# Kernel tuning notes

Measured on AMD Instinct MI355X. Metric: run time of the kernel, lower is better.

The kernel has to match this reference:

```python
import jax, jax.numpy as jnp
import numpy as np

B, S, D, H = 2, 2048, 2048, 16
DH = D // H  # 128


def _rope_tables(seq_len, head_dim, base=10000.0):
    inv_freq = 1.0 / (base ** (jnp.arange(0, head_dim, 2, dtype=jnp.float32) / head_dim))
    t = jnp.arange(seq_len, dtype=jnp.float32)
    freqs = jnp.outer(t, inv_freq)                      # [S, DH/2]
    emb = jnp.concatenate([freqs, freqs], axis=-1)      # [S, DH]
    return jnp.cos(emb), jnp.sin(emb)


def _rotate_half(x):
    x1, x2 = jnp.split(x, 2, axis=-1)
    return jnp.concatenate([-x2, x1], axis=-1)


def setup_inputs() -> dict:
    key = jax.random.key(0)
    ks = jax.random.split(key, 5)
    sc = 0.02
    return {
        "hidden_states": jax.random.normal(ks[0], (B, S, D), jnp.float32),
        "Wq": jax.random.normal(ks[1], (D, D), jnp.float32) * sc,
        "Wk": jax.random.normal(ks[2], (D, D), jnp.float32) * sc,
        "Wv": jax.random.normal(ks[3], (D, D), jnp.float32) * sc,
        "Wo": jax.random.normal(ks[4], (D, D), jnp.float32) * sc,
        "medical_bias": jnp.zeros((1, H, 1, 1), jnp.float32),
    }


def reference(hidden_states, Wq, Wk, Wv, Wo, medical_bias):
    b, s, _ = hidden_states.shape
    # torch Linear: y = x @ W.T  (W is [out, in])
    def proj(x, W):
        y = jnp.einsum('bsd,ed->bse', x, W)
        return y.reshape(b, s, H, DH).transpose(0, 2, 1, 3)  # [b,H,s,DH]

    q = proj(hidden_states, Wq)
    k = proj(hidden_states, Wk)
    v = proj(hidden_states, Wv)

    cos, sin = _rope_tables(s, DH)                 # [s, DH]
    cos = cos[None, None]                          # [1,1,s,DH]
    sin = sin[None, None]
    q = q * cos + _rotate_half(q) * sin
    k = k * cos + _rotate_half(k) * sin

    scores = jnp.einsum('bhqd,bhkd->bhqk', q, k) / jnp.sqrt(jnp.float32(DH))
    scores = scores + medical_bias                 # learned per-head bias
    probs = jax.nn.softmax(scores, axis=-1)
    out = jnp.einsum('bhqk,bhkd->bhqd', probs, v)  # [b,H,s,DH]
    out = out.transpose(0, 2, 1, 3).reshape(b, s, D)
    return jnp.einsum('bsd,ed->bse', out, Wo)
```

## Files before the change

kernel.cpp:

```cpp
#include <hip/hip_runtime.h>
#include <stdint.h>


#define B_ 2
#define S_ 2048
#define D_ 2048
#define H_ 16

typedef float f32x4 __attribute__((ext_vector_type(4)));
typedef short s16x8 __attribute__((ext_vector_type(8)));

__device__ __forceinline__ unsigned short f2bf(float f) {
  union { float f; uint32_t u; } c; c.f = f;
  return (unsigned short)((c.u + 0x7fffu + ((c.u >> 16) & 1u)) >> 16);
}

#define FAST_EXP2(x) __builtin_amdgcn_exp2f(x)

__device__ __forceinline__ void gld_lds16(const void* g, void* l) {
  __builtin_amdgcn_global_load_lds(
      (const __attribute__((address_space(1))) uint32_t*)g,
      (__attribute__((address_space(3))) uint32_t*)l, 16, 0, 0);
}

__global__ __launch_bounds__(256) void k_f2bf_all(
    const float* __restrict__ hs, const float* __restrict__ wq,
    const float* __restrict__ wk, const float* __restrict__ wv,
    const float* __restrict__ wo, unsigned short* __restrict__ hb,
    unsigned short* __restrict__ wall) {
  const int NH = 2097152, NW = 1048576;
  int i = blockIdx.x * 256 + threadIdx.x;
  const int stride = gridDim.x * 256;
  for (; i < NH + 4 * NW; i += stride) {
    f32x4 v;
    ushort4* dst;
    if (i < NH) {
      v = ((const f32x4*)hs)[i];
      dst = (ushort4*)hb + i;
    } else {
      const int j = i - NH;
      const int rgn = j >> 20;
      const int o = j & (NW - 1);
      const float* s = (rgn == 0) ? wq : (rgn == 1) ? wk : (rgn == 2) ? wv : wo;
      v = ((const f32x4*)s)[o];
      dst = (ushort4*)wall + j;
    }
    ushort4 u;
    u.x = f2bf(v.x); u.y = f2bf(v.y); u.z = f2bf(v.z); u.w = f2bf(v.w);
    *dst = u;
  }
}

__global__ __launch_bounds__(256) void k_tab(float2* __restrict__ t2) {
  int t = blockIdx.x * 256 + threadIdx.x;
  int s = t >> 6, j = t & 63;
  float inv = expf(-(float)j * (1.0f / 64.0f) * 9.210340371976184f);
  float sv, cv;
  sincosf((float)s * inv, &sv, &cv);
  t2[t] = float2{cv, sv};
}

__global__ __launch_bounds__(256, 2) void k_gemm(
    const unsigned short* __restrict__ A,
    const unsigned short* __restrict__ W0,
    const unsigned short* __restrict__ W1,
    const unsigned short* __restrict__ W2,
    float* __restrict__ C0,
    unsigned short* __restrict__ Qo,
    unsigned short* __restrict__ Ko,
    unsigned short* __restrict__ VT,
    const float2* __restrict__ tab,
    int plain) {
  __shared__ unsigned short Al[2][128 * 64];
  __shared__ unsigned short Bl[2][128 * 64];

  const int l0 = ((int)blockIdx.z * 32 + (int)blockIdx.y) * 16 + (int)blockIdx.x;
  const int qx = ((int)gridDim.z * 512) >> 3;
  const int wg = (l0 & 7) * qx + (l0 >> 3);
  const int z = wg >> 9;
  const unsigned short* __restrict__ Wp = (z == 0) ? W0 : (z == 1) ? W1 : W2;

  const int tid = threadIdx.x;
  const int w = tid >> 6;
  const int l = tid & 63;
  const int row0 = ((wg >> 4) & 31) * 128;
  const int col0 = (wg & 15) * 128;

  const int c16 = l & 15, g = l >> 4;
  const int cx = c16 & 7;

  const int srow = l >> 3;
  const int sslot = (l & 7) ^ (l >> 3);
  const int scol = sslot << 3;

  int kbase[2];
#pragma unroll
  for (int kk = 0; kk < 2; ++kk)
    kbase[kk] = c16 * 128 + (((kk * 4 + g) ^ cx) << 4);
  const char* AW0 = (const char*)&Al[0][0] + w * 4096;
  const char* AW1 = (const char*)&Al[1][0] + w * 4096;
  const char* BB0 = (const char*)&Bl[0][0];
  const char* BB1 = (const char*)&Bl[1][0];

  f32x4 acc[2][8];
#pragma unroll
  for (int m = 0; m < 2; ++m)
#pragma unroll
    for (int n = 0; n < 8; ++n)
      acc[m][n] = f32x4{0.f, 0.f, 0.f, 0.f};

#define STAGE_G(K0, BUF)                                                       \
  do {                                                                         \
    _Pragma("unroll") for (int i = 0; i < 4; ++i) {                            \
      const int jj = (w << 2) + i;                                             \
      gld_lds16(&A[(size_t)(row0 + (jj << 3) + srow) * 2048 + (K0) + scol],    \
                &Al[BUF][jj * 512]);                                           \
      gld_lds16(&Wp[(size_t)(col0 + (jj << 3) + srow) * 2048 + (K0) + scol],   \
                &Bl[BUF][jj * 512]);                                           \
    }                                                                          \
  } while (0)

#define COMPUTE_G(AW, BBp)                                                     \
  do {                                                                         \
    _Pragma("unroll") for (int kk = 0; kk < 2; ++kk) {                         \
      s16x8 a[2], b[8];                                                        \
      _Pragma("unroll") for (int m = 0; m < 2; ++m)                            \
          a[m] = *(const s16x8*)((AW) + m * 2048 + kbase[kk]);                 \
      _Pragma("unroll") for (int n = 0; n < 8; ++n)                            \
          b[n] = *(const s16x8*)((BBp) + n * 2048 + kbase[kk]);                \
      __builtin_amdgcn_s_setprio(1);                                           \
      _Pragma("unroll") for (int m = 0; m < 2; ++m)                            \
          _Pragma("unroll") for (int n = 0; n < 8; ++n)                        \
              acc[m][n] = __builtin_amdgcn_mfma_f32_16x16x32_bf16(             \
                  a[m], b[n], acc[m][n], 0, 0, 0);                             \
      __builtin_amdgcn_s_setprio(0);                                           \
    }                                                                          \
  } while (0)

  STAGE_G(0, 0);
  __syncthreads();
  for (int k0 = 0; k0 < 2048; k0 += 128) {
    STAGE_G(k0 + 64, 1);
    COMPUTE_G(AW0, BB0);
    __syncthreads();
    if (k0 + 128 < 2048) STAGE_G(k0 + 128, 0);
    COMPUTE_G(AW1, BB1);
    __syncthreads();
  }
#undef STAGE_G
#undef COMPUTE_G

  if (plain) {
#pragma unroll
    for (int m = 0; m < 2; ++m) {
      const int gr = row0 + w * 32 + m * 16 + g * 4;
#pragma unroll
      for (int n = 0; n < 8; ++n) {
        const int gc = col0 + n * 16 + c16;
#pragma unroll
        for (int r = 0; r < 4; ++r)
          C0[(size_t)(gr + r) * 2048 + gc] = acc[m][n][r];
      }
    }
  } else if (z == 2) {
#pragma unroll
    for (int m = 0; m < 2; ++m) {
      const int gr = row0 + w * 32 + m * 16 + g * 4;
      const int b_ = gr >> 11, s_ = gr & 2047;
#pragma unroll
      for (int n = 0; n < 8; ++n) {
        const int gc = col0 + n * 16 + c16;
        ushort4 o;
        o.x = f2bf(acc[m][n][0]);
        o.y = f2bf(acc[m][n][1]);
        o.z = f2bf(acc[m][n][2]);
        o.w = f2bf(acc[m][n][3]);
        *(ushort4*)&VT[((size_t)(b_ * 2048 + gc)) * 2048 + s_] = o;
      }
    }
  } else {
    unsigned short* __restrict__ O = z ? Ko : Qo;
    const float sc = z ? 1.0f : (0.08838834764831845f * 1.4426950408889634f);
#pragma unroll
    for (int m = 0; m < 2; ++m) {
#pragma unroll
      for (int r = 0; r < 4; ++r) {
        const int gr = row0 + w * 32 + m * 16 + g * 4 + r;
        const int s_ = gr & 2047;
#pragma unroll
        for (int n = 0; n < 4; ++n) {
          const float2 f = tab[s_ * 64 + n * 16 + c16];
          const float x1 = acc[m][n][r], x2 = acc[m][n + 4][r];
          O[(size_t)gr * 2048 + col0 + n * 16 + c16] =
              f2bf((x1 * f.x - x2 * f.y) * sc);
          O[(size_t)gr * 2048 + col0 + 64 + n * 16 + c16] =
              f2bf((x2 * f.x + x1 * f.y) * sc);
        }
      }
    }
  }
}

__global__ __launch_bounds__(256, 2) void k_attn(
    const unsigned short* __restrict__ Qb,
    const unsigned short* __restrict__ Kb,
    const unsigned short* __restrict__ Vt,
    unsigned short* __restrict__ Ob) {
  __shared__ unsigned short Kl[2][64 * 128];
  __shared__ unsigned short Vl[2][128 * 64];
  __shared__ unsigned short Pl[4][32 * 64];

  const int l0 = (int)blockIdx.y * 16 + (int)blockIdx.x;
  const int wg = (l0 & 7) * 64 + (l0 >> 3);
  const int bh = wg >> 4;
  const int b = bh >> 4, h = bh & 15;

  const int tid = threadIdx.x, w = tid >> 6, l = tid & 63;
  const int q0 = (wg & 15) * 128 + w * 32;
  const int g = l >> 4, c16 = l & 15;
  const int cx = c16 & 7;

  int kaddr[4], vaddr[2];
#pragma unroll
  for (int kc = 0; kc < 4; ++kc)
    kaddr[kc] = c16 * 256 + ((((kc * 4 + g) ^ cx)) << 4);
#pragma unroll
  for (int kc2 = 0; kc2 < 2; ++kc2)
    vaddr[kc2] = c16 * 128 + ((((kc2 * 4 + g) ^ cx)) << 4);
  const char* PW = (const char*)&Pl[w][0];

  s16x8 qf[2][4];
#pragma unroll
  for (int qq = 0; qq < 2; ++qq)
#pragma unroll
    for (int kc = 0; kc < 4; ++kc)
      qf[qq][kc] = *(const s16x8*)&Qb[(size_t)(b * 2048 + q0 + qq * 16 + c16) * 2048 +
                                      h * 128 + kc * 32 + g * 8];

  f32x4 oacc[2][8];
  float mrow[2][4], lrow[2][4];
#pragma unroll
  for (int qq = 0; qq < 2; ++qq) {
#pragma unroll
    for (int df = 0; df < 8; ++df) oacc[qq][df] = f32x4{0.f, 0.f, 0.f, 0.f};
#pragma unroll
    for (int r = 0; r < 4; ++r) { mrow[qq][r] = -INFINITY; lrow[qq][r] = 0.f; }
  }

#define STAGE(T, BUF)                                                          \
  do {                                                                         \
    _Pragma("unroll") for (int i = 0; i < 4; ++i) {                            \
      const int jj = (w << 2) + i;                                             \
      const int krow = jj * 4 + (l >> 4);                                      \
      const int kslot = (l & 15) ^ (krow & 7);                                 \
      gld_lds16(&Kb[(size_t)(b * 2048 + (T) + krow) * 2048 + h * 128 +        \
                    (kslot << 3)],                                             \
                &Kl[BUF][jj * 512]);                                           \
      const int vrow = jj * 8 + (l >> 3);                                      \
      const int vslot = (l & 7) ^ (vrow & 7);                                  \
      gld_lds16(&Vt[(size_t)(bh * 128 + vrow) * 2048 + (T) + (vslot << 3)],    \
                &Vl[BUF][jj * 512]);                                           \
    }                                                                          \
  } while (0)

#define COMPUTE(BUF_)                                                          \
  do {                                                                         \
    f32x4 sacc[2][4];                                                          \
    _Pragma("unroll") for (int qq = 0; qq < 2; ++qq)                           \
        _Pragma("unroll") for (int n = 0; n < 4; ++n)                          \
            sacc[qq][n] = f32x4{0.f, 0.f, 0.f, 0.f};                           \
    const char* KB = (const char*)&Kl[BUF_][0];                                \
    __builtin_amdgcn_s_setprio(1);                                             \
    _Pragma("unroll") for (int kc = 0; kc < 4; ++kc) {                         \
      s16x8 kb[4];                                                             \
      _Pragma("unroll") for (int n = 0; n < 4; ++n)                            \
          kb[n] = *(const s16x8*)(KB + kaddr[kc] + n * 4096);                  \
      _Pragma("unroll") for (int qq = 0; qq < 2; ++qq)                         \
          _Pragma("unroll") for (int n = 0; n < 4; ++n)                        \
              sacc[qq][n] = __builtin_amdgcn_mfma_f32_16x16x32_bf16(           \
                  qf[qq][kc], kb[n], sacc[qq][n], 0, 0, 0);                    \
    }                                                                          \
    __builtin_amdgcn_s_setprio(0);                                             \
            \
    float mx4[2][4];                                                           \
    float need = 0.f;                                                          \
    _Pragma("unroll") for (int qq = 0; qq < 2; ++qq)                           \
        _Pragma("unroll") for (int r = 0; r < 4; ++r) {                        \
      mx4[qq][r] = fmaxf(fmaxf(sacc[qq][0][r], sacc[qq][1][r]),                \
                         fmaxf(sacc[qq][2][r], sacc[qq][3][r]));               \
      need = fmaxf(need, mx4[qq][r] - mrow[qq][r]);                            \
    }                                                                          \
    if (!__all(need <= 8.0f)) {          \
      _Pragma("unroll") for (int qq = 0; qq < 2; ++qq)                         \
          _Pragma("unroll") for (int r = 0; r < 4; ++r) {                      \
        float mx = mx4[qq][r];                                                 \
        mx = fmaxf(mx, __shfl_xor(mx, 1));                                     \
        mx = fmaxf(mx, __shfl_xor(mx, 2));                                     \
        mx = fmaxf(mx, __shfl_xor(mx, 4));                                     \
        mx = fmaxf(mx, __shfl_xor(mx, 8));                                     \
        float mnew = fmaxf(mrow[qq][r], mx);                                   \
        float alpha = FAST_EXP2(mrow[qq][r] - mnew);                           \
        mrow[qq][r] = mnew;                                                    \
        lrow[qq][r] *= alpha;                                                  \
        _Pragma("unroll") for (int df = 0; df < 8; ++df)                       \
            oacc[qq][df][r] *= alpha;                                          \
      }                                                                        \
    }                                                                          \
    _Pragma("unroll") for (int qq = 0; qq < 2; ++qq) {                         \
      _Pragma("unroll") for (int r = 0; r < 4; ++r) {                          \
        float rs = 0.f;                                                        \
        _Pragma("unroll") for (int n = 0; n < 4; ++n) {                        \
          float p = FAST_EXP2(sacc[qq][n][r] - mrow[qq][r]);                   \
          sacc[qq][n][r] = p;                                                  \
          rs += p;                                                             \
        }                                                                      \
        lrow[qq][r] += rs;                                                     \
      }                                                                        \
      _Pragma("unroll") for (int n = 0; n < 4; ++n)                            \
          _Pragma("unroll") for (int r = 0; r < 4; ++r) {                      \
        const int prow = qq * 16 + g * 4 + r;                                  \
        const int psl = (n * 2 + (c16 >> 3)) ^ (prow & 7);                     \
        Pl[w][prow * 64 + (psl << 3) + (c16 & 7)] = f2bf(sacc[qq][n][r]);      \
      }                                                                        \
    }                                                                          \
    const char* VB = (const char*)&Vl[BUF_][0];                                \
    __builtin_amdgcn_s_setprio(1);                                             \
    _Pragma("unroll") for (int kc2 = 0; kc2 < 2; ++kc2) {                      \
      s16x8 pa[2];                                                             \
      pa[0] = *(const s16x8*)(PW + vaddr[kc2]);                                \
      pa[1] = *(const s16x8*)(PW + vaddr[kc2] + 2048);                         \
      _Pragma("unroll") for (int df = 0; df < 8; ++df) {                       \
        s16x8 vb = *(const s16x8*)(VB + vaddr[kc2] + df * 2048);               \
        oacc[0][df] = __builtin_amdgcn_mfma_f32_16x16x32_bf16(pa[0], vb,       \
                                                              oacc[0][df], 0, 0, 0); \
        oacc[1][df] = __builtin_amdgcn_mfma_f32_16x16x32_bf16(pa[1], vb,       \
                                                              oacc[1][df], 0, 0, 0); \
      }                                                                        \
    }                                                                          \
    __builtin_amdgcn_s_setprio(0);                                             \
  } while (0)

  STAGE(0, 0);
  __syncthreads();
  for (int t = 0; t < 2048; t += 128) {
    STAGE(t + 64, 1);
    COMPUTE(0);
    __syncthreads();
    if (t + 128 < 2048) STAGE(t + 128, 0);
    COMPUTE(1);
    __syncthreads();
  }
#undef STAGE
#undef COMPUTE

#pragma unroll
  for (int qq = 0; qq < 2; ++qq)
#pragma unroll
    for (int r = 0; r < 4; ++r) {
      float tot = lrow[qq][r];
      tot += __shfl_xor(tot, 1);
      tot += __shfl_xor(tot, 2);
      tot += __shfl_xor(tot, 4);
      tot += __shfl_xor(tot, 8);
      const float inv = 1.0f / tot;
      const int srow_ = q0 + qq * 16 + g * 4 + r;
#pragma unroll
      for (int df = 0; df < 8; ++df)
        Ob[(size_t)(b * 2048 + srow_) * 2048 + h * 128 + df * 16 + c16] =
            f2bf(oacc[qq][df][r] * inv);
    }
}

extern "C" void kernel_launch(void* const* d_in, const int* in_sizes, int n_in,
                              void* d_out, int out_size, void* d_ws, size_t ws_size,
                              hipStream_t stream) {
  const float* hs = (const float*)d_in[0];
  const float* Wq = (const float*)d_in[1];
  const float* Wk = (const float*)d_in[2];
  const float* Wv = (const float*)d_in[3];
  const float* Wo = (const float*)d_in[4];
  float* out = (float*)d_out;
  char* ws = (char*)d_ws;

  unsigned short* hb   = (unsigned short*)(ws + 0);
  unsigned short* wall = (unsigned short*)(ws + 16777216);
  unsigned short* wqb  = wall;
  unsigned short* wkb  = wall + 4194304;
  unsigned short* wvb  = wall + 8388608;
  unsigned short* wob  = wall + 12582912;
  unsigned short* Qbb  = (unsigned short*)(ws + 50331648);
  unsigned short* Kbb  = (unsigned short*)(ws + 67108864);
  unsigned short* Vt   = (unsigned short*)(ws + 83886080);
  float2*         tab2 = (float2*)(ws + 100663296);
  unsigned short* Ob   = hb;

  k_f2bf_all<<<2048, 256, 0, stream>>>(hs, Wq, Wk, Wv, Wo, hb, wall);
  k_tab<<<512, 256, 0, stream>>>(tab2);

  k_gemm<<<dim3(16, 32, 3), 256, 0, stream>>>(hb, wqb, wkb, wvb, nullptr, Qbb,
                                              Kbb, Vt, tab2, 0);
  k_attn<<<dim3(16, 32), 256, 0, stream>>>(Qbb, Kbb, Vt, Ob);
  k_gemm<<<dim3(16, 32, 1), 256, 0, stream>>>(Ob, wob, nullptr, nullptr, out,
                                              nullptr, nullptr, nullptr, tab2, 1);
}
```

Baseline: 262.9 us.

## Split attention work across eight waves with sixteen query rows each

The attention kernel moves from 256 threads with 32 query rows per wave to 512 threads with 16 query rows per wave, so each block still covers 128 queries. Each wave holds half the Q fragments, accumulators and softmax state, and the K/V staging loop is split over twice as many waves. The intent is lower register pressure and more resident waves to hide LDS and MFMA latency. In exchange, each K/V fragment loaded from LDS now feeds half as many MFMAs, so LDS read traffic per FLOP doubles, and launch bounds of (512,4) may force register limits.

```diff
diff --git a/kernel.cpp b/kernel.cpp
--- a/kernel.cpp
+++ b/kernel.cpp
@@ -201,14 +201,14 @@
   }
 }
 
-__global__ __launch_bounds__(256, 2) void k_attn(
+__global__ __launch_bounds__(512, 4) void k_attn(
     const unsigned short* __restrict__ Qb,
     const unsigned short* __restrict__ Kb,
     const unsigned short* __restrict__ Vt,
     unsigned short* __restrict__ Ob) {
   __shared__ unsigned short Kl[2][64 * 128];
   __shared__ unsigned short Vl[2][128 * 64];
-  __shared__ unsigned short Pl[4][32 * 64];
+  __shared__ unsigned short Pl[8][16 * 64];
 
   const int l0 = (int)blockIdx.y * 16 + (int)blockIdx.x;
   const int wg = (l0 & 7) * 64 + (l0 >> 3);
@@ -216,7 +216,7 @@
   const int b = bh >> 4, h = bh & 15;
 
   const int tid = threadIdx.x, w = tid >> 6, l = tid & 63;
-  const int q0 = (wg & 15) * 128 + w * 32;
+  const int q0w = (wg & 15) * 128 + w * 16;
   const int g = l >> 4, c16 = l & 15;
   const int cx = c16 & 7;
 
@@ -229,28 +229,23 @@
     vaddr[kc2] = c16 * 128 + ((((kc2 * 4 + g) ^ cx)) << 4);
   const char* PW = (const char*)&Pl[w][0];
 
-  s16x8 qf[2][4];
-#pragma unroll
-  for (int qq = 0; qq < 2; ++qq)
-#pragma unroll
-    for (int kc = 0; kc < 4; ++kc)
-      qf[qq][kc] = *(const s16x8*)&Qb[(size_t)(b * 2048 + q0 + qq * 16 + c16) * 2048 +
-                                      h * 128 + kc * 32 + g * 8];
-
-  f32x4 oacc[2][8];
-  float mrow[2][4], lrow[2][4];
-#pragma unroll
-  for (int qq = 0; qq < 2; ++qq) {
-#pragma unroll
-    for (int df = 0; df < 8; ++df) oacc[qq][df] = f32x4{0.f, 0.f, 0.f, 0.f};
-#pragma unroll
-    for (int r = 0; r < 4; ++r) { mrow[qq][r] = -INFINITY; lrow[qq][r] = 0.f; }
-  }
+  s16x8 qf[4];
+#pragma unroll
+  for (int kc = 0; kc < 4; ++kc)
+    qf[kc] = *(const s16x8*)&Qb[(size_t)(b * 2048 + q0w + c16) * 2048 +
+                                h * 128 + kc * 32 + g * 8];
+
+  f32x4 oacc[8];
+  float mrow[4], lrow[4];
+#pragma unroll
+  for (int df = 0; df < 8; ++df) oacc[df] = f32x4{0.f, 0.f, 0.f, 0.f};
+#pragma unroll
+  for (int r = 0; r < 4; ++r) { mrow[r] = -INFINITY; lrow[r] = 0.f; }
 
 #define STAGE(T, BUF)                                                          \
   do {                                                                         \
-    _Pragma("unroll") for (int i = 0; i < 4; ++i) {                            \
-      const int jj = (w << 2) + i;                                             \
+    _Pragma("unroll") for (int i = 0; i < 2; ++i) {                            \
+      const int jj = (w << 1) + i;                                             \
       const int krow = jj * 4 + (l >> 4);                                      \
       const int kslot = (l & 15) ^ (krow & 7);                                 \
       gld_lds16(&Kb[(size_t)(b * 2048 + (T) + krow) * 2048 + h * 128 +        \
@@ -265,76 +260,66 @@
 
 #define COMPUTE(BUF_)                                                          \
   do {                                                                         \
-    f32x4 sacc[2][4];                                                          \
-    _Pragma("unroll") for (int qq = 0; qq < 2; ++qq)                           \
-        _Pragma("unroll") for (int n = 0; n < 4; ++n)                          \
-            sacc[qq][n] = f32x4{0.f, 0.f, 0.f, 0.f};                           \
+    f32x4 sacc[4];                                                             \
+    _Pragma("unroll") for (int n = 0; n < 4; ++n)                              \
+        sacc[n] = f32x4{0.f, 0.f, 0.f, 0.f};                                   \
     const char* KB = (const char*)&Kl[BUF_][0];                                \
     __builtin_amdgcn_s_setprio(1);                                             \
     _Pragma("unroll") for (int kc = 0; kc < 4; ++kc) {                         \
       s16x8 kb[4];                                                             \
       _Pragma("unroll") for (int n = 0; n < 4; ++n)                            \
           kb[n] = *(const s16x8*)(KB + kaddr[kc] + n * 4096);                  \
-      _Pragma("unroll") for (int qq = 0; qq < 2; ++qq)                         \
-          _Pragma("unroll") for (int n = 0; n < 4; ++n)                        \
-              sacc[qq][n] = __builtin_amdgcn_mfma_f32_16x16x32_bf16(           \
-                  qf[qq][kc], kb[n], sacc[qq][n], 0, 0, 0);                    \
+      _Pragma("unroll") for (int n = 0; n < 4; ++n)                            \
+          sacc[n] = __builtin_amdgcn_mfma_f32_16x16x32_bf16(                   \
+              qf[kc], kb[n], sacc[n], 0, 0, 0);                                \
     }                                                                          \
     __builtin_amdgcn_s_setprio(0);                                             \
             \
-    float mx4[2][4];                                                           \
+    float mx4[4];                                                              \
     float need = 0.f;                                                          \
-    _Pragma("unroll") for (int qq = 0; qq < 2; ++qq)                           \
-        _Pragma("unroll") for (int r = 0; r < 4; ++r) {                        \
-      mx4[qq][r] = fmaxf(fmaxf(sacc[qq][0][r], sacc[qq][1][r]),                \
-                         fmaxf(sacc[qq][2][r], sacc[qq][3][r]));               \
-      need = fmaxf(need, mx4[qq][r] - mrow[qq][r]);                            \
+    _Pragma("unroll") for (int r = 0; r < 4; ++r) {                            \
+      mx4[r] = fmaxf(fmaxf(sacc[0][r], sacc[1][r]),                            \
+                     fmaxf(sacc[2][r], sacc[3][r]));                           \
+      need = fmaxf(need, mx4[r] - mrow[r]);                                    \
     }                                                                          \
     if (!__all(need <= 8.0f)) {          \
-      _Pragma("unroll") for (int qq = 0; qq < 2; ++qq)                         \
-          _Pragma("unroll") for (int r = 0; r < 4; ++r) {                      \
-        float mx = mx4[qq][r];                                                 \
+      _Pragma("unroll") for (int r = 0; r < 4; ++r) {                          \
+        float mx = mx4[r];                                                     \
         mx = fmaxf(mx, __shfl_xor(mx, 1));                                     \
         mx = fmaxf(mx, __shfl_xor(mx, 2));                                     \
         mx = fmaxf(mx, __shfl_xor(mx, 4));                                     \
         mx = fmaxf(mx, __shfl_xor(mx, 8));                                     \
-        float mnew = fmaxf(mrow[qq][r], mx);                                   \
-        float alpha = FAST_EXP2(mrow[qq][r] - mnew);                           \
-        mrow[qq][r] = mnew;                                                    \
-        lrow[qq][r] *= alpha;                                                  \
+        float mnew = fmaxf(mrow[r], mx);                                       \
+        float alpha = FAST_EXP2(mrow[r] - mnew);                               \
+        mrow[r] = mnew;                                                        \
+        lrow[r] *= alpha;                                                      \
         _Pragma("unroll") for (int df = 0; df < 8; ++df)                       \
-            oacc[qq][df][r] *= alpha;                                          \
+            oacc[df][r] *= alpha;                                              \
       }                                                                        \
     }                                                                          \
-    _Pragma("unroll") for (int qq = 0; qq < 2; ++qq) {                         \
-      _Pragma("unroll") for (int r = 0; r < 4; ++r) {                          \
-        float rs = 0.f;                                                        \
-        _Pragma("unroll") for (int n = 0; n < 4; ++n) {                        \
-          float p = FAST_EXP2(sacc[qq][n][r] - mrow[qq][r]);                   \
-          sacc[qq][n][r] = p;                                                  \
-          rs += p;                                                             \
-        }                                                                      \
-        lrow[qq][r] += rs;                                                     \
+    _Pragma("unroll") for (int r = 0; r < 4; ++r) {                            \
+      float rs = 0.f;                                                          \
+      _Pragma("unroll") for (int n = 0; n < 4; ++n) {                          \
+        float p = FAST_EXP2(sacc[n][r] - mrow[r]);                             \
+        sacc[n][r] = p;                                                        \
+        rs += p;                                                               \
       }                                                                        \
-      _Pragma("unroll") for (int n = 0; n < 4; ++n)                            \
-          _Pragma("unroll") for (int r = 0; r < 4; ++r) {                      \
-        const int prow = qq * 16 + g * 4 + r;                                  \
-        const int psl = (n * 2 + (c16 >> 3)) ^ (prow & 7);                     \
-        Pl[w][prow * 64 + (psl << 3) + (c16 & 7)] = f2bf(sacc[qq][n][r]);      \
-      }                                                                        \
+      lrow[r] += rs;                                                           \
+    }                                                                          \
+    _Pragma("unroll") for (int n = 0; n < 4; ++n)                              \
+        _Pragma("unroll") for (int r = 0; r < 4; ++r) {                        \
+      const int prow = g * 4 + r;                                              \
+      const int psl = (n * 2 + (c16 >> 3)) ^ (prow & 7);                       \
+      Pl[w][prow * 64 + (psl << 3) + (c16 & 7)] = f2bf(sacc[n][r]);            \
     }                                                                          \
     const char* VB = (const char*)&Vl[BUF_][0];                                \
     __builtin_amdgcn_s_setprio(1);                                             \
     _Pragma("unroll") for (int kc2 = 0; kc2 < 2; ++kc2) {                      \
-      s16x8 pa[2];                                                             \
-      pa[0] = *(const s16x8*)(PW + vaddr[kc2]);                                \
-      pa[1] = *(const s16x8*)(PW + vaddr[kc2] + 2048);                         \
+      s16x8 pa = *(const s16x8*)(PW + vaddr[kc2]);                             \
       _Pragma("unroll") for (int df = 0; df < 8; ++df) {                       \
         s16x8 vb = *(const s16x8*)(VB + vaddr[kc2] + df * 2048);               \
-        oacc[0][df] = __builtin_amdgcn_mfma_f32_16x16x32_bf16(pa[0], vb,       \
-                                                              oacc[0][df], 0, 0, 0); \
-        oacc[1][df] = __builtin_amdgcn_mfma_f32_16x16x32_bf16(pa[1], vb,       \
-                                                              oacc[1][df], 0, 0, 0); \
+        oacc[df] = __builtin_amdgcn_mfma_f32_16x16x32_bf16(pa, vb,             \
+                                                           oacc[df], 0, 0, 0); \
       }                                                                        \
     }                                                                          \
     __builtin_amdgcn_s_setprio(0);                                             \
@@ -354,21 +339,19 @@
 #undef COMPUTE
 
 #pragma unroll
-  for (int qq = 0; qq < 2; ++qq)
-#pragma unroll
-    for (int r = 0; r < 4; ++r) {
-      float tot = lrow[qq][r];
-      tot += __shfl_xor(tot, 1);
-      tot += __shfl_xor(tot, 2);
-      tot += __shfl_xor(tot, 4);
-      tot += __shfl_xor(tot, 8);
-      const float inv = 1.0f / tot;
-      const int srow_ = q0 + qq * 16 + g * 4 + r;
-#pragma unroll
-      for (int df = 0; df < 8; ++df)
-        Ob[(size_t)(b * 2048 + srow_) * 2048 + h * 128 + df * 16 + c16] =
-            f2bf(oacc[qq][df][r] * inv);
-    }
+  for (int r = 0; r < 4; ++r) {
+    float tot = lrow[r];
+    tot += __shfl_xor(tot, 1);
+    tot += __shfl_xor(tot, 2);
+    tot += __shfl_xor(tot, 4);
+    tot += __shfl_xor(tot, 8);
+    const float inv = 1.0f / tot;
+    const int srow_ = q0w + g * 4 + r;
+#pragma unroll
+    for (int df = 0; df < 8; ++df)
+      Ob[(size_t)(b * 2048 + srow_) * 2048 + h * 128 + df * 16 + c16] =
+          f2bf(oacc[df][r] * inv);
+  }
 }
 
 extern "C" void kernel_launch(void* const* d_in, const int* in_sizes, int n_in,
@@ -399,7 +382,7 @@
 
   k_gemm<<<dim3(16, 32, 3), 256, 0, stream>>>(hb, wqb, wkb, wvb, nullptr, Qbb,
                                               Kbb, Vt, tab2, 0);
-  k_attn<<<dim3(16, 32), 256, 0, stream>>>(Qbb, Kbb, Vt, Ob);
+  k_attn<<<dim3(16, 32), 512, 0, stream>>>(Qbb, Kbb, Vt, Ob);
   k_gemm<<<dim3(16, 32, 1), 256, 0, stream>>>(Ob, wob, nullptr, nullptr, out,
                                               nullptr, nullptr, nullptr, tab2, 1);
 }
```

Measured after the change: 283.3 us. 1.08x slower.
